# Kernel optimization log

Hardware: AMD Instinct MI355X
Metric: run time of the kernel (lower is better)

Reference implementation:

```python
import jax, jax.numpy as jnp
import numpy as np

B, N, D, H, W = 8, 4096, 256, 64, 64  # N must equal H*W for the Z normalization einsum


def setup_inputs() -> dict:
    key = jax.random.key(0)
    ks = jax.random.split(key, 10)
    s = 1.0 / np.sqrt(D)
    return {
        "query": jax.random.normal(ks[0], (B, N, D), jnp.float32),
        "key_value": jax.random.normal(ks[1], (B, D, H, W), jnp.float32),
        "Wq": jax.random.uniform(ks[2], (D, D), jnp.float32, -s, s),
        "bq": jax.random.uniform(ks[3], (D,), jnp.float32, -s, s),
        "Wk": jax.random.uniform(ks[4], (D, D), jnp.float32, -s, s),
        "bk": jax.random.uniform(ks[5], (D,), jnp.float32, -s, s),
        "Wv": jax.random.uniform(ks[6], (D, D), jnp.float32, -s, s),
        "bv": jax.random.uniform(ks[7], (D,), jnp.float32, -s, s),
        "Wo": jax.random.uniform(ks[8], (D, D), jnp.float32, -s, s),
        "bo": jax.random.uniform(ks[9], (D,), jnp.float32, -s, s),
    }


def reference(query, key_value, Wq, bq, Wk, bk, Wv, bv, Wo, bo):
    b, n, d = query.shape
    # [B, C, H, W] -> [B, HW, C]
    kv_flat = key_value.reshape(b, d, -1).transpose(0, 2, 1)
    # projections (torch Linear: x @ W.T + b) fused with elu+1 feature maps
    Q = jax.nn.elu(jnp.einsum('bnd,ed->bne', query, Wq) + bq) + 1.0   # [B, N, D]
    K = jax.nn.elu(jnp.einsum('bmd,ed->bme', kv_flat, Wk) + bk) + 1.0  # [B, HW, D]
    V = jnp.einsum('bmd,ed->bme', kv_flat, Wv) + bv                    # [B, HW, D]
    # KV outer-product accumulation over kv tokens
    KV = jnp.einsum('bmc,bmd->bcd', K, V)                              # [B, D, D]
    # Z[b,m] = sum_c K[b,m,c]  (used per-token; requires N == HW)
    Z = K.sum(axis=-1)                                                 # [B, N]
    num = jnp.einsum('bnc,bcd->bnd', Q, KV)                            # [B, N, D]
    den = Q.sum(axis=-1) * Z                                           # [B, N]
    out = num / (den[..., None] + 1e-6)
    return jnp.einsum('bnd,ed->bne', out, Wo) + bo
```

## Files before the change

### kernel.cpp

```cpp
#include <hip/hip_runtime.h>
#include <hip/hip_bf16.h>


typedef __attribute__((ext_vector_type(8))) __bf16 bf16x8;
typedef __attribute__((ext_vector_type(4))) float f32x4;
typedef __attribute__((ext_vector_type(4))) unsigned short u16x4;
typedef __attribute__((ext_vector_type(8))) unsigned short u16x8;

#define DEVI __device__ __forceinline__

static constexpr int BATCH = 8;
static constexpr int NTOK  = 4096;
static constexpr int DDIM  = 256;

DEVI float bf2f(unsigned short u) {
  union { float f; unsigned int i; } x; x.i = ((unsigned int)u) << 16; return x.f;
}
DEVI unsigned short f2bf(float f) {
  union { float f; unsigned int i; } x; x.f = f;
  unsigned int r = x.i + 0x7fffu + ((x.i >> 16) & 1u);
  return (unsigned short)(r >> 16);
}

__global__ __launch_bounds__(256) void conv_q_kernel(const float* __restrict__ src,
                                                     unsigned short* __restrict__ dst) {
  size_t base = ((size_t)blockIdx.x * 256 + threadIdx.x) * 16;
#pragma unroll
  for (int j = 0; j < 4; ++j) {
    float4 v = *reinterpret_cast<const float4*>(src + base + j * 4);
    u16x4 o = { f2bf(v.x), f2bf(v.y), f2bf(v.z), f2bf(v.w) };
    *reinterpret_cast<u16x4*>(dst + base + j * 4) = o;
  }
}

__global__ __launch_bounds__(256) void conv_w_kernel(const float* __restrict__ w0, const float* __restrict__ w1,
                                                     const float* __restrict__ w2, const float* __restrict__ w3,
                                                     unsigned short* __restrict__ o0, unsigned short* __restrict__ o1,
                                                     unsigned short* __restrict__ o2, unsigned short* __restrict__ o3) {
  size_t i = ((size_t)blockIdx.x * 256 + threadIdx.x) * 4;
  float4 a = *reinterpret_cast<const float4*>(w0 + i);
  float4 b = *reinterpret_cast<const float4*>(w1 + i);
  float4 c = *reinterpret_cast<const float4*>(w2 + i);
  float4 d = *reinterpret_cast<const float4*>(w3 + i);
  u16x4 oa = { f2bf(a.x), f2bf(a.y), f2bf(a.z), f2bf(a.w) };
  u16x4 ob = { f2bf(b.x), f2bf(b.y), f2bf(b.z), f2bf(b.w) };
  u16x4 oc = { f2bf(c.x), f2bf(c.y), f2bf(c.z), f2bf(c.w) };
  u16x4 od = { f2bf(d.x), f2bf(d.y), f2bf(d.z), f2bf(d.w) };
  *reinterpret_cast<u16x4*>(o0 + i) = oa;
  *reinterpret_cast<u16x4*>(o1 + i) = ob;
  *reinterpret_cast<u16x4*>(o2 + i) = oc;
  *reinterpret_cast<u16x4*>(o3 + i) = od;
}

__global__ __launch_bounds__(256) void kv_transpose(const float* __restrict__ src,
                                                    unsigned short* __restrict__ dst) {
  __shared__ float t[32][33];
  int b = blockIdx.z;
  int m0 = blockIdx.x * 32, d0 = blockIdx.y * 32;
  int tx = threadIdx.x, ty = threadIdx.y;
  const float* s = src + ((size_t)b * DDIM + d0) * NTOK + m0;
#pragma unroll
  for (int i = 0; i < 4; ++i) t[ty + i * 8][tx] = s[(size_t)(ty + i * 8) * NTOK + tx];
  __syncthreads();
  unsigned short* d = dst + ((size_t)b * NTOK + m0) * DDIM + d0;
#pragma unroll
  for (int i = 0; i < 4; ++i) d[(size_t)(ty + i * 8) * DDIM + tx] = f2bf(t[tx][ty + i * 8]);
}

__global__ __launch_bounds__(256) void t64_kernel(const unsigned short* __restrict__ src,
                                                  unsigned short* __restrict__ dst) {
  constexpr int LDT = 68;
  __shared__ unsigned short Ts[64 * LDT];
  const int tid = threadIdx.x;
  const int b = blockIdx.z;
  const int m0 = blockIdx.x * 64;
  const int c0 = blockIdx.y * 64;
  {
    const int cg = tid & 15;
    const int rb = tid >> 4;
#pragma unroll
    for (int it = 0; it < 4; ++it) {
      int r = rb + it * 16;
      u16x4 v = *reinterpret_cast<const u16x4*>(src + ((size_t)b * NTOK + m0 + r) * 256 + c0 + cg * 4);
      *reinterpret_cast<u16x4*>(&Ts[r * LDT + cg * 4]) = v;
    }
  }
  __syncthreads();
  {
    const int c = tid >> 2;
    const int mg = tid & 3;
    u16x8 o0, o1;
#pragma unroll
    for (int j = 0; j < 8; ++j) o0[j] = Ts[(mg * 16 + j) * LDT + c];
#pragma unroll
    for (int j = 0; j < 8; ++j) o1[j] = Ts[(mg * 16 + 8 + j) * LDT + c];
    unsigned short* d = dst + ((size_t)b * DDIM + c0 + c) * NTOK + m0 + mg * 16;
    *reinterpret_cast<u16x8*>(d) = o0;
    *reinterpret_cast<u16x8*>(d + 8) = o1;
  }
}

template <int ACT, int OUTF32>
__global__ __launch_bounds__(256) void gemm_proj(const unsigned short* __restrict__ A,
                                                 const unsigned short* __restrict__ W,
                                                 const float* __restrict__ bias,
                                                 void* __restrict__ outp) {
  constexpr int LDT = 72;
  __shared__ unsigned short As[128 * LDT];
  __shared__ unsigned short Ws[128 * LDT];

  const int tid = threadIdx.x;
  const int m0 = blockIdx.x * 128;
  const int c0 = blockIdx.y * 128;
  const int w = tid >> 6, l = tid & 63;
  const int wr = (w >> 1) * 64, wc = (w & 1) * 64;
  const int lr = l & 15, lk = (l >> 4) * 8;

  f32x4 acc[4][4] = {};

  for (int k0 = 0; k0 < 256; k0 += 64) {
#pragma unroll
    for (int it = 0; it < 4; ++it) {
      int idx = tid + it * 256;
      int r = idx >> 3;
      int c = (idx & 7) * 8;
      *reinterpret_cast<u16x8*>(&As[r * LDT + c]) =
          *reinterpret_cast<const u16x8*>(A + (size_t)(m0 + r) * 256 + k0 + c);
      *reinterpret_cast<u16x8*>(&Ws[r * LDT + c]) =
          *reinterpret_cast<const u16x8*>(W + (size_t)(c0 + r) * 256 + k0 + c);
    }
    __syncthreads();
#pragma unroll
    for (int kk = 0; kk < 2; ++kk) {
      bf16x8 a[4], b[4];
#pragma unroll
      for (int m = 0; m < 4; ++m)
        a[m] = *reinterpret_cast<const bf16x8*>(&As[(wr + m * 16 + lr) * LDT + kk * 32 + lk]);
#pragma unroll
      for (int n = 0; n < 4; ++n)
        b[n] = *reinterpret_cast<const bf16x8*>(&Ws[(wc + n * 16 + lr) * LDT + kk * 32 + lk]);
#pragma unroll
      for (int m = 0; m < 4; ++m)
#pragma unroll
        for (int n = 0; n < 4; ++n)
          acc[m][n] = __builtin_amdgcn_mfma_f32_16x16x32_bf16(a[m], b[n], acc[m][n], 0, 0, 0);
    }
    __syncthreads();
  }

#pragma unroll
  for (int n = 0; n < 4; ++n) {
    const int col = c0 + wc + n * 16 + lr;
    const float bv = bias[col];
#pragma unroll
    for (int m = 0; m < 4; ++m) {
#pragma unroll
      for (int j = 0; j < 4; ++j) {
        int row = m0 + wr + m * 16 + (l >> 4) * 4 + j;
        float x = acc[m][n][j] + bv;
        if (ACT) x = (x > 0.0f) ? (x + 1.0f) : __expf(x);
        if (OUTF32)
          reinterpret_cast<float*>(outp)[(size_t)row * 256 + col] = x;
        else
          reinterpret_cast<unsigned short*>(outp)[(size_t)row * 256 + col] = f2bf(x);
      }
    }
  }
}

__global__ __launch_bounds__(256) void den_kernel(const unsigned short* __restrict__ Qb,
                                                  const unsigned short* __restrict__ Kb,
                                                  float* __restrict__ den) {
  int row = blockIdx.x * 4 + (threadIdx.x >> 6);
  int l = threadIdx.x & 63;
  u16x4 q = *reinterpret_cast<const u16x4*>(Qb + (size_t)row * 256 + l * 4);
  u16x4 k = *reinterpret_cast<const u16x4*>(Kb + (size_t)row * 256 + l * 4);
  float qs = bf2f(q[0]) + bf2f(q[1]) + bf2f(q[2]) + bf2f(q[3]);
  float ks = bf2f(k[0]) + bf2f(k[1]) + bf2f(k[2]) + bf2f(k[3]);
#pragma unroll
  for (int s = 32; s > 0; s >>= 1) {
    qs += __shfl_xor(qs, s);
    ks += __shfl_xor(ks, s);
  }
  if (l == 0) den[row] = qs * ks;
}

__global__ __launch_bounds__(256) void kv_gemm(const unsigned short* __restrict__ Vt,
                                               const unsigned short* __restrict__ Kt,
                                               float* __restrict__ partial) {
  constexpr int LDT = 72;
  __shared__ unsigned short As[128 * LDT];
  __shared__ unsigned short Bs[128 * LDT];
  const int tid = threadIdx.x;
  const int b = blockIdx.z;
  const int s = blockIdx.y;
  const int c0 = (blockIdx.x & 1) * 128;
  const int d0 = (blockIdx.x >> 1) * 128;
  const int ms = s * 512;

  const int w = tid >> 6, l = tid & 63;
  const int wr = (w >> 1) * 64, wc = (w & 1) * 64;
  const int lr = l & 15, lk = (l >> 4) * 8;

  const size_t vbase = ((size_t)b * DDIM + d0) * NTOK;
  const size_t kbase = ((size_t)b * DDIM + c0) * NTOK;

  f32x4 acc[4][4] = {};

  for (int mc = 0; mc < 512; mc += 64) {
#pragma unroll
    for (int it = 0; it < 4; ++it) {
      int idx = tid + it * 256;
      int r = idx >> 3;
      int kg = (idx & 7) * 8;
      *reinterpret_cast<u16x8*>(&As[r * LDT + kg]) =
          *reinterpret_cast<const u16x8*>(Vt + vbase + (size_t)r * NTOK + ms + mc + kg);
      *reinterpret_cast<u16x8*>(&Bs[r * LDT + kg]) =
          *reinterpret_cast<const u16x8*>(Kt + kbase + (size_t)r * NTOK + ms + mc + kg);
    }
    __syncthreads();
#pragma unroll
    for (int kk = 0; kk < 2; ++kk) {
      bf16x8 a[4], bb[4];
#pragma unroll
      for (int m = 0; m < 4; ++m)
        a[m] = *reinterpret_cast<const bf16x8*>(&As[(wr + m * 16 + lr) * LDT + kk * 32 + lk]);
#pragma unroll
      for (int n = 0; n < 4; ++n)
        bb[n] = *reinterpret_cast<const bf16x8*>(&Bs[(wc + n * 16 + lr) * LDT + kk * 32 + lk]);
#pragma unroll
      for (int m = 0; m < 4; ++m)
#pragma unroll
        for (int n = 0; n < 4; ++n)
          acc[m][n] = __builtin_amdgcn_mfma_f32_16x16x32_bf16(a[m], bb[n], acc[m][n], 0, 0, 0);
    }
    __syncthreads();
  }

  float* p = partial + (size_t)(s * BATCH + b) * 65536;
#pragma unroll
  for (int n = 0; n < 4; ++n) {
    int c = c0 + wc + n * 16 + lr;
#pragma unroll
    for (int m = 0; m < 4; ++m) {
#pragma unroll
      for (int j = 0; j < 4; ++j) {
        int d = d0 + wr + m * 16 + (l >> 4) * 4 + j;
        p[(size_t)d * 256 + c] = acc[m][n][j];
      }
    }
  }
}

__global__ __launch_bounds__(256) void kv_reduce(const float* __restrict__ partial,
                                                 float* __restrict__ KVT) {
  size_t i = ((size_t)blockIdx.x * 256 + threadIdx.x) * 4;
  float4 acc = *reinterpret_cast<const float4*>(partial + i);
#pragma unroll
  for (int s = 1; s < 8; ++s) {
    float4 v = *reinterpret_cast<const float4*>(partial + (size_t)s * 524288 + i);
    acc.x += v.x; acc.y += v.y; acc.z += v.z; acc.w += v.w;
  }
  *reinterpret_cast<float4*>(KVT + i) = acc;
}

__global__ __launch_bounds__(256) void gemm_num(const unsigned short* __restrict__ Qb,
                                                const float* __restrict__ KVT,
                                                const float* __restrict__ den,
                                                unsigned short* __restrict__ outb) {
  constexpr int LDT = 72;
  __shared__ unsigned short As[128 * LDT];
  __shared__ unsigned short Bs[128 * LDT];
  const int tid = threadIdx.x;
  const int b = blockIdx.z;
  const int m0 = blockIdx.x * 128;
  const int d0 = blockIdx.y * 128;
  const size_t abase = (size_t)b * NTOK;

  const int w = tid >> 6, l = tid & 63;
  const int wr = (w >> 1) * 64, wc = (w & 1) * 64;
  const int lr = l & 15, lk = (l >> 4) * 8;

  f32x4 acc[4][4] = {};

  for (int k0 = 0; k0 < 256; k0 += 64) {
#pragma unroll
    for (int it = 0; it < 4; ++it) {
      int idx = tid + it * 256;
      int r = idx >> 3, c = (idx & 7) * 8;
      *reinterpret_cast<u16x8*>(&As[r * LDT + c]) =
          *reinterpret_cast<const u16x8*>(Qb + (abase + m0 + r) * 256 + k0 + c);
    }
#pragma unroll
    for (int it = 0; it < 8; ++it) {
      int idx = tid + it * 256;
      int dl = idx >> 4;
      int cl = (idx & 15) * 4;
      float4 v = *reinterpret_cast<const float4*>(KVT + ((size_t)b * 256 + d0 + dl) * 256 + k0 + cl);
      u16x4 o = { f2bf(v.x), f2bf(v.y), f2bf(v.z), f2bf(v.w) };
      *reinterpret_cast<u16x4*>(&Bs[dl * LDT + cl]) = o;
    }
    __syncthreads();
#pragma unroll
    for (int kk = 0; kk < 2; ++kk) {
      bf16x8 a[4], bb[4];
#pragma unroll
      for (int m = 0; m < 4; ++m)
        a[m] = *reinterpret_cast<const bf16x8*>(&As[(wr + m * 16 + lr) * LDT + kk * 32 + lk]);
#pragma unroll
      for (int n = 0; n < 4; ++n)
        bb[n] = *reinterpret_cast<const bf16x8*>(&Bs[(wc + n * 16 + lr) * LDT + kk * 32 + lk]);
#pragma unroll
      for (int m = 0; m < 4; ++m)
#pragma unroll
        for (int n = 0; n < 4; ++n)
          acc[m][n] = __builtin_amdgcn_mfma_f32_16x16x32_bf16(a[m], bb[n], acc[m][n], 0, 0, 0);
    }
    __syncthreads();
  }

#pragma unroll
  for (int n = 0; n < 4; ++n) {
    int col = d0 + wc + n * 16 + lr;
#pragma unroll
    for (int m = 0; m < 4; ++m) {
#pragma unroll
      for (int j = 0; j < 4; ++j) {
        int row = m0 + wr + m * 16 + (l >> 4) * 4 + j;
        float dv = den[abase + row] + 1e-6f;
        outb[(abase + row) * 256 + col] = f2bf(acc[m][n][j] / dv);
      }
    }
  }
}

extern "C" void kernel_launch(void* const* d_in, const int* in_sizes, int n_in,
                              void* d_out, int out_size, void* d_ws, size_t ws_size,
                              hipStream_t stream) {
  const float* query     = (const float*)d_in[0];
  const float* key_value = (const float*)d_in[1];
  const float* Wq = (const float*)d_in[2];
  const float* bq = (const float*)d_in[3];
  const float* Wk = (const float*)d_in[4];
  const float* bk = (const float*)d_in[5];
  const float* Wv = (const float*)d_in[6];
  const float* bv = (const float*)d_in[7];
  const float* Wo = (const float*)d_in[8];
  const float* bo = (const float*)d_in[9];

  char* ws = (char*)d_ws;
  const size_t MB = 1ull << 20;
  unsigned short* q_bf  = (unsigned short*)(ws + 0 * MB);
  unsigned short* kv_bf = (unsigned short*)(ws + 16 * MB);
  unsigned short* Qb    = (unsigned short*)(ws + 32 * MB);
  unsigned short* Kb    = (unsigned short*)(ws + 48 * MB);
  unsigned short* Vb    = (unsigned short*)(ws + 64 * MB);
  float* KVT            = (float*)(ws + 80 * MB);
  float* den            = (float*)(ws + 82 * MB);
  unsigned short* wqb   = (unsigned short*)(ws + 82 * MB + 128 * 1024);
  unsigned short* wkb   = (unsigned short*)(ws + 82 * MB + 256 * 1024);
  unsigned short* wvb   = (unsigned short*)(ws + 82 * MB + 384 * 1024);
  unsigned short* wob   = (unsigned short*)(ws + 82 * MB + 512 * 1024);
  unsigned short* Kt    = q_bf;
  unsigned short* Vt    = kv_bf;
  float* partial        = (float*)(ws + 64 * MB);
  unsigned short* outb  = q_bf;

  conv_q_kernel<<<2048, 256, 0, stream>>>(query, q_bf);
  conv_w_kernel<<<64, 256, 0, stream>>>(Wq, Wk, Wv, Wo, wqb, wkb, wvb, wob);
  kv_transpose<<<dim3(128, 8, 8), dim3(32, 8), 0, stream>>>(key_value, kv_bf);

  gemm_proj<1, 0><<<dim3(256, 2), 256, 0, stream>>>(q_bf, wqb, bq, Qb);
  gemm_proj<1, 0><<<dim3(256, 2), 256, 0, stream>>>(kv_bf, wkb, bk, Kb);
  gemm_proj<0, 0><<<dim3(256, 2), 256, 0, stream>>>(kv_bf, wvb, bv, Vb);

  t64_kernel<<<dim3(64, 4, 8), 256, 0, stream>>>(Kb, Kt);
  t64_kernel<<<dim3(64, 4, 8), 256, 0, stream>>>(Vb, Vt);

  den_kernel<<<8192, 256, 0, stream>>>(Qb, Kb, den);
  kv_gemm<<<dim3(4, 8, 8), 256, 0, stream>>>(Vt, Kt, partial);
  kv_reduce<<<512, 256, 0, stream>>>(partial, KVT);

  gemm_num<<<dim3(32, 2, 8), 256, 0, stream>>>(Qb, KVT, den, outb);
  gemm_proj<0, 1><<<dim3(256, 2), 256, 0, stream>>>(outb, wob, bo, d_out);
}
```

Measured before the change: 255.3 us.

## Fold output projection into per-batch KV matrix to drop the final token GEMM

Reassociates (Q·KV)·Wo^T as Q·(KV·Wo^T). The per-batch 256x256 product Wo·KV^T is computed once in a small new GEMM, and the final kernel applies it directly to Q with the denominator scaling and bias fused in. This removes one full token-sized GEMM and the bf16 intermediate round trip through memory. It also stores KV in bf16 instead of fp32 and adds an extra bf16 rounding of the combined matrix, which may slightly change numerics.

Result: no change. 256.5 us (+0.4%).

```diff
diff --git a/kernel.cpp b/kernel.cpp
--- a/kernel.cpp
+++ b/kernel.cpp
@@ -100,11 +100,11 @@
   }
 }
 
-template <int ACT, int OUTF32>
+template <int ACT>
 __global__ __launch_bounds__(256) void gemm_proj(const unsigned short* __restrict__ A,
                                                  const unsigned short* __restrict__ W,
                                                  const float* __restrict__ bias,
-                                                 void* __restrict__ outp) {
+                                                 unsigned short* __restrict__ outp) {
   constexpr int LDT = 72;
   __shared__ unsigned short As[128 * LDT];
   __shared__ unsigned short Ws[128 * LDT];
@@ -159,10 +159,7 @@
         int row = m0 + wr + m * 16 + (l >> 4) * 4 + j;
         float x = acc[m][n][j] + bv;
         if (ACT) x = (x > 0.0f) ? (x + 1.0f) : __expf(x);
-        if (OUTF32)
-          reinterpret_cast<float*>(outp)[(size_t)row * 256 + col] = x;
-        else
-          reinterpret_cast<unsigned short*>(outp)[(size_t)row * 256 + col] = f2bf(x);
+        outp[(size_t)row * 256 + col] = f2bf(x);
       }
     }
   }
@@ -185,8 +182,8 @@
   if (l == 0) den[row] = qs * ks;
 }
 
-__global__ __launch_bounds__(256) void kv_gemm(const unsigned short* __restrict__ Vt,
-                                               const unsigned short* __restrict__ Kt,
+__global__ __launch_bounds__(256) void kv_gemm(const unsigned short* __restrict__ Kt,
+                                               const unsigned short* __restrict__ Vt,
                                                float* __restrict__ partial) {
   constexpr int LDT = 72;
   __shared__ unsigned short As[128 * LDT];
@@ -194,16 +191,16 @@
   const int tid = threadIdx.x;
   const int b = blockIdx.z;
   const int s = blockIdx.y;
-  const int c0 = (blockIdx.x & 1) * 128;
-  const int d0 = (blockIdx.x >> 1) * 128;
+  const int ct0 = (blockIdx.x >> 1) * 128;
+  const int dt0 = (blockIdx.x & 1) * 128;
   const int ms = s * 512;
 
   const int w = tid >> 6, l = tid & 63;
   const int wr = (w >> 1) * 64, wc = (w & 1) * 64;
   const int lr = l & 15, lk = (l >> 4) * 8;
 
-  const size_t vbase = ((size_t)b * DDIM + d0) * NTOK;
-  const size_t kbase = ((size_t)b * DDIM + c0) * NTOK;
+  const size_t kbase = ((size_t)b * DDIM + ct0) * NTOK;
+  const size_t vbase = ((size_t)b * DDIM + dt0) * NTOK;
 
   f32x4 acc[4][4] = {};
 
@@ -214,9 +211,9 @@
       int r = idx >> 3;
       int kg = (idx & 7) * 8;
       *reinterpret_cast<u16x8*>(&As[r * LDT + kg]) =
+          *reinterpret_cast<const u16x8*>(Kt + kbase + (size_t)r * NTOK + ms + mc + kg);
+      *reinterpret_cast<u16x8*>(&Bs[r * LDT + kg]) =
           *reinterpret_cast<const u16x8*>(Vt + vbase + (size_t)r * NTOK + ms + mc + kg);
-      *reinterpret_cast<u16x8*>(&Bs[r * LDT + kg]) =
-          *reinterpret_cast<const u16x8*>(Kt + kbase + (size_t)r * NTOK + ms + mc + kg);
     }
     __syncthreads();
 #pragma unroll
@@ -240,20 +237,20 @@
   float* p = partial + (size_t)(s * BATCH + b) * 65536;
 #pragma unroll
   for (int n = 0; n < 4; ++n) {
-    int c = c0 + wc + n * 16 + lr;
+    int d = dt0 + wc + n * 16 + lr;
 #pragma unroll
     for (int m = 0; m < 4; ++m) {
 #pragma unroll
       for (int j = 0; j < 4; ++j) {
-        int d = d0 + wr + m * 16 + (l >> 4) * 4 + j;
-        p[(size_t)d * 256 + c] = acc[m][n][j];
+        int c = ct0 + wr + m * 16 + (l >> 4) * 4 + j;
+        p[(size_t)c * 256 + d] = acc[m][n][j];
       }
     }
   }
 }
 
 __global__ __launch_bounds__(256) void kv_reduce(const float* __restrict__ partial,
-                                                 float* __restrict__ KVT) {
+                                                 unsigned short* __restrict__ KVb) {
   size_t i = ((size_t)blockIdx.x * 256 + threadIdx.x) * 4;
   float4 acc = *reinterpret_cast<const float4*>(partial + i);
 #pragma unroll
@@ -261,21 +258,87 @@
     float4 v = *reinterpret_cast<const float4*>(partial + (size_t)s * 524288 + i);
     acc.x += v.x; acc.y += v.y; acc.z += v.z; acc.w += v.w;
   }
-  *reinterpret_cast<float4*>(KVT + i) = acc;
-}
-
-__global__ __launch_bounds__(256) void gemm_num(const unsigned short* __restrict__ Qb,
-                                                const float* __restrict__ KVT,
-                                                const float* __restrict__ den,
-                                                unsigned short* __restrict__ outb) {
+  u16x4 o = { f2bf(acc.x), f2bf(acc.y), f2bf(acc.z), f2bf(acc.w) };
+  *reinterpret_cast<u16x4*>(KVb + i) = o;
+}
+
+__global__ __launch_bounds__(256) void w2_gemm(const unsigned short* __restrict__ wob,
+                                               const unsigned short* __restrict__ KVb,
+                                               unsigned short* __restrict__ W2T) {
+  constexpr int LDT = 72;
+  __shared__ unsigned short As[128 * LDT];
+  __shared__ unsigned short Bs[128 * LDT];
+  const int tid = threadIdx.x;
+  const int b = blockIdx.z;
+  const int e0 = blockIdx.x * 128;
+  const int c0 = blockIdx.y * 128;
+  const unsigned short* Bsrc = KVb + (size_t)b * 65536;
+
+  const int w = tid >> 6, l = tid & 63;
+  const int wr = (w >> 1) * 64, wc = (w & 1) * 64;
+  const int lr = l & 15, lk = (l >> 4) * 8;
+
+  f32x4 acc[4][4] = {};
+
+  for (int k0 = 0; k0 < 256; k0 += 64) {
+#pragma unroll
+    for (int it = 0; it < 4; ++it) {
+      int idx = tid + it * 256;
+      int r = idx >> 3;
+      int c = (idx & 7) * 8;
+      *reinterpret_cast<u16x8*>(&As[r * LDT + c]) =
+          *reinterpret_cast<const u16x8*>(wob + (size_t)(e0 + r) * 256 + k0 + c);
+      *reinterpret_cast<u16x8*>(&Bs[r * LDT + c]) =
+          *reinterpret_cast<const u16x8*>(Bsrc + (size_t)(c0 + r) * 256 + k0 + c);
+    }
+    __syncthreads();
+#pragma unroll
+    for (int kk = 0; kk < 2; ++kk) {
+      bf16x8 a[4], bb[4];
+#pragma unroll
+      for (int m = 0; m < 4; ++m)
+        a[m] = *reinterpret_cast<const bf16x8*>(&As[(wr + m * 16 + lr) * LDT + kk * 32 + lk]);
+#pragma unroll
+      for (int n = 0; n < 4; ++n)
+        bb[n] = *reinterpret_cast<const bf16x8*>(&Bs[(wc + n * 16 + lr) * LDT + kk * 32 + lk]);
+#pragma unroll
+      for (int m = 0; m < 4; ++m)
+#pragma unroll
+        for (int n = 0; n < 4; ++n)
+          acc[m][n] = __builtin_amdgcn_mfma_f32_16x16x32_bf16(a[m], bb[n], acc[m][n], 0, 0, 0);
+    }
+    __syncthreads();
+  }
+
+  unsigned short* out = W2T + (size_t)b * 65536;
+#pragma unroll
+  for (int n = 0; n < 4; ++n) {
+    int c = c0 + wc + n * 16 + lr;
+#pragma unroll
+    for (int m = 0; m < 4; ++m) {
+#pragma unroll
+      for (int j = 0; j < 4; ++j) {
+        int e = e0 + wr + m * 16 + (l >> 4) * 4 + j;
+        out[(size_t)e * 256 + c] = f2bf(acc[m][n][j]);
+      }
+    }
+  }
+}
+
+__global__ __launch_bounds__(256) void gemm_final(const unsigned short* __restrict__ Qb,
+                                                  const unsigned short* __restrict__ W2T,
+                                                  const float* __restrict__ den,
+                                                  const float* __restrict__ bo,
+                                                  float* __restrict__ outp) {
   constexpr int LDT = 72;
   __shared__ unsigned short As[128 * LDT];
   __shared__ unsigned short Bs[128 * LDT];
   const int tid = threadIdx.x;
   const int b = blockIdx.z;
   const int m0 = blockIdx.x * 128;
-  const int d0 = blockIdx.y * 128;
+  const int e0 = blockIdx.y * 128;
   const size_t abase = (size_t)b * NTOK;
+  const unsigned short* Bsrc = W2T + (size_t)b * 65536;
 
   const int w = tid >> 6, l = tid & 63;
   const int wr = (w >> 1) * 64, wc = (w & 1) * 64;
@@ -290,15 +353,8 @@
       int r = idx >> 3, c = (idx & 7) * 8;
       *reinterpret_cast<u16x8*>(&As[r * LDT + c]) =
           *reinterpret_cast<const u16x8*>(Qb + (abase + m0 + r) * 256 + k0 + c);
-    }
-#pragma unroll
-    for (int it = 0; it < 8; ++it) {
-      int idx = tid + it * 256;
-      int dl = idx >> 4;
-      int cl = (idx & 15) * 4;
-      float4 v = *reinterpret_cast<const float4*>(KVT + ((size_t)b * 256 + d0 + dl) * 256 + k0 + cl);
-      u16x4 o = { f2bf(v.x), f2bf(v.y), f2bf(v.z), f2bf(v.w) };
-      *reinterpret_cast<u16x4*>(&Bs[dl * LDT + cl]) = o;
+      *reinterpret_cast<u16x8*>(&Bs[r * LDT + c]) =
+          *reinterpret_cast<const u16x8*>(Bsrc + (size_t)(e0 + r) * 256 + k0 + c);
     }
     __syncthreads();
 #pragma unroll
@@ -321,14 +377,15 @@
 
 #pragma unroll
   for (int n = 0; n < 4; ++n) {
-    int col = d0 + wc + n * 16 + lr;
+    int col = e0 + wc + n * 16 + lr;
+    const float bv = bo[col];
 #pragma unroll
     for (int m = 0; m < 4; ++m) {
 #pragma unroll
       for (int j = 0; j < 4; ++j) {
         int row = m0 + wr + m * 16 + (l >> 4) * 4 + j;
         float dv = den[abase + row] + 1e-6f;
-        outb[(abase + row) * 256 + col] = f2bf(acc[m][n][j] / dv);
+        outp[(abase + row) * 256 + col] = acc[m][n][j] / dv + bv;
       }
     }
   }
@@ -355,7 +412,8 @@
   unsigned short* Qb    = (unsigned short*)(ws + 32 * MB);
   unsigned short* Kb    = (unsigned short*)(ws + 48 * MB);
   unsigned short* Vb    = (unsigned short*)(ws + 64 * MB);
-  float* KVT            = (float*)(ws + 80 * MB);
+  unsigned short* KVb   = (unsigned short*)(ws + 80 * MB);
+  unsigned short* W2T   = (unsigned short*)(ws + 81 * MB);
   float* den            = (float*)(ws + 82 * MB);
   unsigned short* wqb   = (unsigned short*)(ws + 82 * MB + 128 * 1024);
   unsigned short* wkb   = (unsigned short*)(ws + 82 * MB + 256 * 1024);
@@ -364,23 +422,22 @@
   unsigned short* Kt    = q_bf;
   unsigned short* Vt    = kv_bf;
   float* partial        = (float*)(ws + 64 * MB);
-  unsigned short* outb  = q_bf;
 
   conv_q_kernel<<<2048, 256, 0, stream>>>(query, q_bf);
   conv_w_kernel<<<64, 256, 0, stream>>>(Wq, Wk, Wv, Wo, wqb, wkb, wvb, wob);
   kv_transpose<<<dim3(128, 8, 8), dim3(32, 8), 0, stream>>>(key_value, kv_bf);
 
-  gemm_proj<1, 0><<<dim3(256, 2), 256, 0, stream>>>(q_bf, wqb, bq, Qb);
-  gemm_proj<1, 0><<<dim3(256, 2), 256, 0, stream>>>(kv_bf, wkb, bk, Kb);
-  gemm_proj<0, 0><<<dim3(256, 2), 256, 0, stream>>>(kv_bf, wvb, bv, Vb);
+  gemm_proj<1><<<dim3(256, 2), 256, 0, stream>>>(q_bf, wqb, bq, Qb);
+  gemm_proj<1><<<dim3(256, 2), 256, 0, stream>>>(kv_bf, wkb, bk, Kb);
+  gemm_proj<0><<<dim3(256, 2), 256, 0, stream>>>(kv_bf, wvb, bv, Vb);
 
   t64_kernel<<<dim3(64, 4, 8), 256, 0, stream>>>(Kb, Kt);
   t64_kernel<<<dim3(64, 4, 8), 256, 0, stream>>>(Vb, Vt);
 
   den_kernel<<<8192, 256, 0, stream>>>(Qb, Kb, den);
-  kv_gemm<<<dim3(4, 8, 8), 256, 0, stream>>>(Vt, Kt, partial);
-  kv_reduce<<<512, 256, 0, stream>>>(partial, KVT);
-
-  gemm_num<<<dim3(32, 2, 8), 256, 0, stream>>>(Qb, KVT, den, outb);
-  gemm_proj<0, 1><<<dim3(256, 2), 256, 0, stream>>>(outb, wob, bo, d_out);
-}
+  kv_gemm<<<dim3(4, 8, 8), 256, 0, stream>>>(Kt, Vt, partial);
+  kv_reduce<<<512, 256, 0, stream>>>(partial, KVb);
+  w2_gemm<<<dim3(2, 2, 8), 256, 0, stream>>>(wob, KVb, W2T);
+
+  gemm_final<<<dim3(32, 2, 8), 256, 0, stream>>>(Qb, W2T, den, bo, (float*)d_out);
+}
```
